# Performance work log

Measured on AMD Instinct MI355X. Metric: run time of the kernel, lower is better.

## Reference

```python
import jax, jax.numpy as jnp
import numpy as np

DIM = 3072
HEADS = 24
HEAD_DIM = 128
MLP_HIDDEN = 12288
SEQ = 2048
BATCH = 1
EPS = 1e-6


def setup_inputs() -> dict:
    key = jax.random.key(0)
    ks = jax.random.split(key, 12)
    s = 0.02
    return {
        "hidden_states": jax.random.normal(ks[0], (BATCH, SEQ, DIM), jnp.float32),
        "temb": jax.random.normal(ks[1], (BATCH, DIM), jnp.float32),
        "rope_cos": jax.random.uniform(ks[2], (SEQ, HEAD_DIM), jnp.float32),
        "rope_sin": jax.random.uniform(ks[3], (SEQ, HEAD_DIM), jnp.float32),
        # AdaLN-Zero single: Linear(dim -> 3*dim)
        "norm_w": jax.random.normal(ks[4], (3 * DIM, DIM), jnp.float32) * s,
        "norm_b": jnp.zeros((3 * DIM,), jnp.float32),
        # fused QKV + MLP projection: Linear(dim -> 3*dim + mlp_hidden)
        "qkv_mlp_w": jax.random.normal(ks[5], (3 * DIM + MLP_HIDDEN, DIM), jnp.float32) * s,
        "qkv_mlp_b": jnp.zeros((3 * DIM + MLP_HIDDEN,), jnp.float32),
        # proj_out: Linear(dim + mlp_hidden -> dim)
        "proj_w": jax.random.normal(ks[6], (DIM, DIM + MLP_HIDDEN), jnp.float32) * s,
        "proj_b": jnp.zeros((DIM,), jnp.float32),
        # qk RMSNorm weights (per head_dim)
        "rms_q_w": jnp.ones((HEAD_DIM,), jnp.float32),
        "rms_k_w": jnp.ones((HEAD_DIM,), jnp.float32),
    }


def _rms_norm(x, w):
    # x: [B,S,H,D], normalize over D
    var = jnp.mean(jnp.square(x), axis=-1, keepdims=True)
    return x * jax.lax.rsqrt(var + EPS) * w


def _apply_rope(x, cos, sin):
    # x: [B,S,H,D]; cos/sin: [S,D]. diffusers use_real, unbind_dim=-1 convention.
    xr = x.reshape(*x.shape[:-1], HEAD_DIM // 2, 2)
    rot = jnp.stack([-xr[..., 1], xr[..., 0]], axis=-1).reshape(x.shape)
    c = cos[None, :, None, :]
    s = sin[None, :, None, :]
    return x * c + rot * s


def reference(hidden_states, temb, rope_cos, rope_sin, norm_w, norm_b,
              qkv_mlp_w, qkv_mlp_b, proj_w, proj_b, rms_q_w, rms_k_w):
    B, S, _ = hidden_states.shape
    residual = hidden_states

    # --- AdaLayerNormZeroSingle ---
    mod = jax.nn.silu(temb) @ norm_w.T + norm_b          # [B, 3*dim]
    shift, scale, gate = jnp.split(mod, 3, axis=-1)       # each [B, dim]
    mu = jnp.mean(hidden_states, axis=-1, keepdims=True)
    var = jnp.mean(jnp.square(hidden_states - mu), axis=-1, keepdims=True)
    ln = (hidden_states - mu) * jax.lax.rsqrt(var + EPS)
    norm_h = ln * (1.0 + scale[:, None, :]) + shift[:, None, :]

    # --- fused QKV + MLP GEMM ---
    qkv_mlp = norm_h @ qkv_mlp_w.T + qkv_mlp_b             # [B,S,3*dim+mlp]
    qkv, mlp_h = jnp.split(qkv_mlp, [3 * DIM], axis=-1)
    mlp_out = jax.nn.gelu(mlp_h, approximate=True)         # tanh GELU

    q, k, v = jnp.split(qkv, 3, axis=-1)
    q = q.reshape(B, S, HEADS, HEAD_DIM)
    k = k.reshape(B, S, HEADS, HEAD_DIM)
    v = v.reshape(B, S, HEADS, HEAD_DIM)

    # qk RMSNorm + RoPE
    q = _apply_rope(_rms_norm(q, rms_q_w), rope_cos, rope_sin)
    k = _apply_rope(_rms_norm(k, rms_k_w), rope_cos, rope_sin)

    # scaled dot-product attention
    scale_f = 1.0 / np.sqrt(HEAD_DIM)
    scores = jnp.einsum("bqhd,bkhd->bhqk", q, k) * scale_f
    probs = jax.nn.softmax(scores, axis=-1)
    attn = jnp.einsum("bhqk,bkhd->bqhd", probs, v).reshape(B, S, DIM)

    # proj_out on concat(attn, gelu(mlp)) + gated residual
    cat = jnp.concatenate([attn, mlp_out], axis=-1)        # [B,S,dim+mlp]
    proj = cat @ proj_w.T + proj_b                          # [B,S,dim]
    return gate[:, None, :] * proj + residual
```

## Files before the change

### kernel.cpp

```cpp
#include <hip/hip_runtime.h>
#include <stdint.h>

typedef __bf16 bf16;
typedef __bf16 bf16x8 __attribute__((ext_vector_type(8)));
typedef __bf16 bf16x4 __attribute__((ext_vector_type(4)));
typedef float f32x4 __attribute__((ext_vector_type(4)));

#define DIM   3072
#define SEQ   2048
#define QKVW  9216
#define MLPH  12288
#define FUSED 21504
#define CATW  15360
#define HD    128
#define NH    24

__device__ __forceinline__ void gload_lds16(const void* g, void* l) {
  __builtin_amdgcn_global_load_lds((__attribute__((address_space(1))) void*)g,
                                   (__attribute__((address_space(3))) void*)l,
                                   16, 0, 0);
}

__global__ __launch_bounds__(256) void k_mod_gemv(
    const float* __restrict__ temb, const float* __restrict__ nw,
    const float* __restrict__ nb, float* __restrict__ mod)
{
  int j = blockIdx.x * 4 + (threadIdx.x >> 6);
  int lane = threadIdx.x & 63;
  const float* row = nw + (size_t)j * DIM;
  float acc = 0.f;
  #pragma unroll
  for (int k0 = 0; k0 < DIM; k0 += 256) {
    int k = k0 + lane * 4;
    float4 w = *(const float4*)(row + k);
    float4 t = *(const float4*)(temb + k);
    float s0 = t.x / (1.f + __expf(-t.x));
    float s1 = t.y / (1.f + __expf(-t.y));
    float s2 = t.z / (1.f + __expf(-t.z));
    float s3 = t.w / (1.f + __expf(-t.w));
    acc += w.x * s0 + w.y * s1 + w.z * s2 + w.w * s3;
  }
  #pragma unroll
  for (int m = 32; m >= 1; m >>= 1) acc += __shfl_xor(acc, m, 64);
  if (lane == 0) mod[j] = acc + nb[j];
}

__global__ __launch_bounds__(256) void k_ln_mod(
    const float* __restrict__ hs, const float* __restrict__ mod,
    bf16* __restrict__ nh)
{
  int m = blockIdx.x;
  int t = threadIdx.x;
  const float* x = hs + (size_t)m * DIM;
  float4 v[3];
  float s = 0.f, ss = 0.f;
  #pragma unroll
  for (int i = 0; i < 3; i++) {
    v[i] = *(const float4*)(x + i * 1024 + t * 4);
    s  += v[i].x + v[i].y + v[i].z + v[i].w;
    ss += v[i].x * v[i].x + v[i].y * v[i].y + v[i].z * v[i].z + v[i].w * v[i].w;
  }
  #pragma unroll
  for (int msk = 32; msk >= 1; msk >>= 1) {
    s  += __shfl_xor(s, msk, 64);
    ss += __shfl_xor(ss, msk, 64);
  }
  __shared__ float red[8];
  int wave = t >> 6;
  if ((t & 63) == 0) { red[wave] = s; red[4 + wave] = ss; }
  __syncthreads();
  s  = red[0] + red[1] + red[2] + red[3];
  ss = red[4] + red[5] + red[6] + red[7];
  float mu  = s * (1.f / DIM);
  float var = ss * (1.f / DIM) - mu * mu;
  float rstd = rsqrtf(var + 1e-6f);
  #pragma unroll
  for (int i = 0; i < 3; i++) {
    int col = i * 1024 + t * 4;
    const float* sc = mod + DIM + col;
    const float* sh = mod + col;
    float4 vv = v[i];
    bf16x4 o;
    o[0] = (bf16)((vv.x - mu) * rstd * (1.f + sc[0]) + sh[0]);
    o[1] = (bf16)((vv.y - mu) * rstd * (1.f + sc[1]) + sh[1]);
    o[2] = (bf16)((vv.z - mu) * rstd * (1.f + sc[2]) + sh[2]);
    o[3] = (bf16)((vv.w - mu) * rstd * (1.f + sc[3]) + sh[3]);
    *(bf16x4*)(nh + (size_t)m * DIM + col) = o;
  }
}

__global__ __launch_bounds__(256) void k_cvt(
    const float* __restrict__ s, bf16* __restrict__ d, size_t n)
{
  size_t stride = (size_t)gridDim.x * 256 * 8;
  for (size_t i = ((size_t)blockIdx.x * 256 + threadIdx.x) * 8; i < n; i += stride) {
    float4 a = *(const float4*)(s + i);
    float4 b = *(const float4*)(s + i + 4);
    bf16x8 h;
    h[0] = (bf16)a.x; h[1] = (bf16)a.y; h[2] = (bf16)a.z; h[3] = (bf16)a.w;
    h[4] = (bf16)b.x; h[5] = (bf16)b.y; h[6] = (bf16)b.z; h[7] = (bf16)b.w;
    *(bf16x8*)(d + i) = h;
  }
}

#define MFMA_B16(a, b, c) __builtin_amdgcn_mfma_f32_16x16x32_bf16(a, b, c, 0, 0, 0)

template<int MODE>
__global__ __launch_bounds__(512, 2) void k_gemm8(
    const bf16* __restrict__ A, const bf16* __restrict__ B,
    const float* __restrict__ bias, int K, int ntn, int nkp,
    bf16* __restrict__ oq, bf16* __restrict__ ocat, float* __restrict__ pk)
{
  __shared__ bf16 lds[65536];
  int tid = threadIdx.x;
  int wave = tid >> 6, lane = tid & 63;
  int wm = wave >> 2, wn = wave & 3;

  int nwg = gridDim.x;
  int bid = blockIdx.x;
  int swz = (bid & 7) * (nwg >> 3) + (bid >> 3);
  int mt = swz & 7;
  int rest = swz >> 3;
  int nt = rest % ntn;
  int kc = rest / ntn;
  int m0 = mt * 256, n0 = nt * 256;
  int Kp = K / nkp;
  int kbeg = kc * Kp;
  int NT = Kp >> 6;

  const bf16* Ag = A + (size_t)m0 * K + kbeg;
  const bf16* Bg = B + (size_t)n0 * K + kbeg;

  int aoffs[2][2], boffs[2][2];
  int aldc[2][2], bldc[2][2];
  #pragma unroll
  for (int q = 0; q < 2; q++) {
    #pragma unroll
    for (int j = 0; j < 2; j++) {
      int ca = j * 16 + q * 8 + wave;
      aoffs[q][j] = ((ca >> 1) * 16 + (lane & 15)) * K + (ca & 1) * 32 + (lane >> 4) * 8;
      aldc[q][j] = ca * 512;
      int v = j * 8 + wave;
      int cb = (v >> 2) * 8 + q * 4 + (v & 3);
      boffs[q][j] = ((cb >> 1) * 16 + (lane & 15)) * K + (cb & 1) * 32 + (lane >> 4) * 8;
      bldc[q][j] = 16384 + cb * 512;
    }
  }

  auto stA = [&](int kt, int q) {
    int kw = kt >= NT ? kt - NT : kt;
    int bo = (kt & 1) << 15;
    gload_lds16(Ag + aoffs[q][0] + kw * 64, &lds[bo + aldc[q][0]]);
    gload_lds16(Ag + aoffs[q][1] + kw * 64, &lds[bo + aldc[q][1]]);
  };
  auto stB = [&](int kt, int q) {
    int kw = kt >= NT ? kt - NT : kt;
    int bo = (kt & 1) << 15;
    gload_lds16(Bg + boffs[q][0] + kw * 64, &lds[bo + bldc[q][0]]);
    gload_lds16(Bg + boffs[q][1] + kw * 64, &lds[bo + bldc[q][1]]);
  };

  f32x4 acc[8][4];
  #pragma unroll
  for (int i = 0; i < 8; i++)
    #pragma unroll
    for (int j = 0; j < 4; j++) acc[i][j] = (f32x4){0.f, 0.f, 0.f, 0.f};

  const int abase = wm * 8192;
  const int bbase = 16384 + wn * 4096;
  const int lo = lane * 8;
  bf16x8 aLo[4][2], aHi[4][2], bLo[2][2], bHi[2][2];

  #define RD_ALO(BO) \
    _Pragma("unroll") for (int mi = 0; mi < 4; mi++) \
    _Pragma("unroll") for (int ks = 0; ks < 2; ks++) \
      aLo[mi][ks] = *(const bf16x8*)&lds[(BO) + abase + (mi * 2 + ks) * 512 + lo];
  #define RD_AHI(BO) \
    _Pragma("unroll") for (int mi = 0; mi < 4; mi++) \
    _Pragma("unroll") for (int ks = 0; ks < 2; ks++) \
      aHi[mi][ks] = *(const bf16x8*)&lds[(BO) + abase + ((4 + mi) * 2 + ks) * 512 + lo];
  #define RD_BLO(BO) \
    _Pragma("unroll") for (int ni = 0; ni < 2; ni++) \
    _Pragma("unroll") for (int ks = 0; ks < 2; ks++) \
      bLo[ni][ks] = *(const bf16x8*)&lds[(BO) + bbase + (ni * 2 + ks) * 512 + lo];
  #define RD_BHI(BO) \
    _Pragma("unroll") for (int ni = 0; ni < 2; ni++) \
    _Pragma("unroll") for (int ks = 0; ks < 2; ks++) \
      bHi[ni][ks] = *(const bf16x8*)&lds[(BO) + bbase + ((2 + ni) * 2 + ks) * 512 + lo];
  #define QUAD(AF, BF, MI0, NI0) \
    __builtin_amdgcn_s_setprio(1); \
    _Pragma("unroll") for (int mi = 0; mi < 4; mi++) \
    _Pragma("unroll") for (int ni = 0; ni < 2; ni++) \
    _Pragma("unroll") for (int ks = 0; ks < 2; ks++) \
      acc[MI0 + mi][NI0 + ni] = MFMA_B16(AF[mi][ks], BF[ni][ks], acc[MI0 + mi][NI0 + ni]); \
    __builtin_amdgcn_s_setprio(0);
  #define BAR()   __builtin_amdgcn_s_barrier()
  #define VM6()   asm volatile("s_waitcnt vmcnt(6)" ::: "memory")

  stA(0, 0); stB(0, 0); stA(0, 1); stB(0, 1);
  stA(1, 0); stB(1, 0); stA(1, 1);
  VM6();
  BAR();
  RD_ALO(0) RD_BLO(0)

  for (int it = 0; it < NT; it += 2) {
    int ta = it, tb = it + 1;
    BAR();
    stB(tb, 1);
    RD_AHI(0)
    QUAD(aLo, bLo, 0, 0)
    BAR();
    stA(ta + 2, 0);
    RD_BHI(0)
    QUAD(aHi, bLo, 4, 0)
    BAR();
    stB(ta + 2, 0);
    QUAD(aLo, bHi, 0, 2)
    stA(ta + 2, 1);
    VM6();
    BAR();
    RD_ALO(32768) RD_BLO(32768)
    QUAD(aHi, bHi, 4, 2)
    BAR();
    stB(ta + 2, 1);
    RD_AHI(32768)
    QUAD(aLo, bLo, 0, 0)
    BAR();
    stA(tb + 2, 0);
    RD_BHI(32768)
    QUAD(aHi, bLo, 4, 0)
    BAR();
    stB(tb + 2, 0);
    QUAD(aLo, bHi, 0, 2)
    stA(tb + 2, 1);
    VM6();
    BAR();
    RD_ALO(0) RD_BLO(0)
    QUAD(aHi, bHi, 4, 2)
  }

  int rr = (lane >> 4) * 4, cl = lane & 15;
  int mw0 = m0 + wm * 128, nw0 = n0 + wn * 64;
  #pragma unroll
  for (int mi = 0; mi < 8; mi++) {
    #pragma unroll
    for (int ni = 0; ni < 4; ni++) {
      int n = nw0 + ni * 16 + cl;
      #pragma unroll
      for (int r = 0; r < 4; r++) {
        int m = mw0 + mi * 16 + rr + r;
        float v = acc[mi][ni][r];
        if (MODE == 0) {
          v += bias[n];
          if (n < QKVW) {
            oq[(size_t)m * QKVW + n] = (bf16)v;
          } else {
            float g = 0.5f * v * (1.f + tanhf(0.7978845608028654f * (v + 0.044715f * v * v * v)));
            ocat[(size_t)m * CATW + DIM + (n - QKVW)] = (bf16)g;
          }
        } else {
          pk[(size_t)kc * SEQ * DIM + (size_t)m * DIM + n] = v;
        }
      }
    }
  }
  #undef RD_ALO
  #undef RD_AHI
  #undef RD_BLO
  #undef RD_BHI
  #undef QUAD
  #undef BAR
  #undef VM6
}

template<int MODE>
__global__ __launch_bounds__(256) void k_gemm2(
    const bf16* __restrict__ A, const float* __restrict__ Bf,
    const float* __restrict__ bias, int K, int ntn,
    bf16* __restrict__ oq, bf16* __restrict__ ocat,
    const float* __restrict__ gate, const float* __restrict__ resid,
    float* __restrict__ of)
{
  __shared__ bf16 sA[8192];
  __shared__ bf16 sB[8192];
  int nwg = gridDim.x;
  int bid = blockIdx.x;
  int swz = (bid & 7) * (nwg >> 3) + (bid >> 3);
  int mt = swz & 15, nt = swz >> 4;
  int m0 = mt * 128, n0 = nt * 128;
  int tid = threadIdx.x;
  int wave = tid >> 6, lane = tid & 63;
  int wr = wave >> 1, wc = wave & 1;

  size_t aoff[4], boff[4];
  bf16* la[4];
  bf16* lb[4];
  #pragma unroll
  for (int i = 0; i < 4; i++) {
    int c = wave * 4 + i;
    int rt = c >> 1, kt = c & 1;
    int row = rt * 16 + (lane & 15);
    int col = kt * 32 + (lane >> 4) * 8;
    aoff[i] = (size_t)(m0 + row) * K + col;
    boff[i] = (size_t)(n0 + row) * K + col;
    la[i] = sA + c * 512;
    lb[i] = sB + c * 512;
  }
  f32x4 acc[4][4];
  #pragma unroll
  for (int i = 0; i < 4; i++)
    #pragma unroll
    for (int j = 0; j < 4; j++) acc[i][j] = (f32x4){0.f, 0.f, 0.f, 0.f};

  for (int kk = 0; kk < K; kk += 64) {
    #pragma unroll
    for (int i = 0; i < 4; i++)
      gload_lds16(A + aoff[i] + kk, la[i]);
    #pragma unroll
    for (int i = 0; i < 4; i++) {
      const float* g = Bf + boff[i] + kk;
      float4 f0 = *(const float4*)g;
      float4 f1 = *(const float4*)(g + 4);
      bf16x8 h;
      h[0] = (bf16)f0.x; h[1] = (bf16)f0.y; h[2] = (bf16)f0.z; h[3] = (bf16)f0.w;
      h[4] = (bf16)f1.x; h[5] = (bf16)f1.y; h[6] = (bf16)f1.z; h[7] = (bf16)f1.w;
      *(bf16x8*)(lb[i] + lane * 8) = h;
    }
    __syncthreads();
    #pragma unroll
    for (int ks = 0; ks < 2; ks++) {
      bf16x8 af[4], bfr[4];
      #pragma unroll
      for (int mi = 0; mi < 4; mi++)
        af[mi] = *(const bf16x8*)(sA + ((wr * 4 + mi) * 2 + ks) * 512 + lane * 8);
      #pragma unroll
      for (int nj = 0; nj < 4; nj++)
        bfr[nj] = *(const bf16x8*)(sB + ((wc * 4 + nj) * 2 + ks) * 512 + lane * 8);
      #pragma unroll
      for (int mi = 0; mi < 4; mi++)
        #pragma unroll
        for (int nj = 0; nj < 4; nj++)
          acc[mi][nj] = __builtin_amdgcn_mfma_f32_16x16x32_bf16(af[mi], bfr[nj], acc[mi][nj], 0, 0, 0);
    }
    __syncthreads();
  }

  int rr = (lane >> 4) * 4;
  int cl = lane & 15;
  #pragma unroll
  for (int mi = 0; mi < 4; mi++) {
    #pragma unroll
    for (int nj = 0; nj < 4; nj++) {
      int mbase = m0 + wr * 64 + mi * 16 + rr;
      int n = n0 + wc * 64 + nj * 16 + cl;
      #pragma unroll
      for (int r = 0; r < 4; r++) {
        int m = mbase + r;
        float v = acc[mi][nj][r] + bias[n];
        if (MODE == 0) {
          if (n < QKVW) {
            oq[(size_t)m * QKVW + n] = (bf16)v;
          } else {
            float g = 0.5f * v * (1.f + tanhf(0.7978845608028654f * (v + 0.044715f * v * v * v)));
            ocat[(size_t)m * CATW + DIM + (n - QKVW)] = (bf16)g;
          }
        } else {
          of[(size_t)m * DIM + n] = gate[n] * v + resid[(size_t)m * DIM + n];
        }
      }
    }
  }
}

__global__ __launch_bounds__(256) void k_red(
    const float* __restrict__ pk, const float* __restrict__ bias,
    const float* __restrict__ gate, const float* __restrict__ resid,
    float* __restrict__ out)
{
  int m = blockIdx.x / 3;
  int n = (blockIdx.x % 3) * 1024 + threadIdx.x * 4;
  size_t idx = (size_t)m * DIM + n;
  f32x4 p0 = *(const f32x4*)(pk + idx);
  f32x4 p1 = *(const f32x4*)(pk + (size_t)SEQ * DIM + idx);
  f32x4 b  = *(const f32x4*)(bias + n);
  f32x4 g  = *(const f32x4*)(gate + n);
  f32x4 r  = *(const f32x4*)(resid + idx);
  f32x4 o;
  #pragma unroll
  for (int i = 0; i < 4; i++) o[i] = g[i] * (p0[i] + p1[i] + b[i]) + r[i];
  *(f32x4*)(out + idx) = o;
}

__global__ __launch_bounds__(256) void k_rmsrope(
    bf16* __restrict__ qkv, const float* __restrict__ rc, const float* __restrict__ rs,
    const float* __restrict__ qw, const float* __restrict__ kw)
{
  int srow = blockIdx.x >> 1;
  int isk  = blockIdx.x & 1;
  int off  = isk ? DIM : 0;
  const float* w = isk ? kw : qw;
  int g = threadIdx.x >> 5, gl = threadIdx.x & 31;
  int d = gl * 4;
  #pragma unroll
  for (int hh = 0; hh < 3; hh++) {
    int h = g + hh * 8;
    bf16* p = qkv + (size_t)srow * QKVW + off + h * HD + d;
    bf16x4 u = *(const bf16x4*)p;
    float x0 = (float)u[0], x1 = (float)u[1], x2 = (float)u[2], x3 = (float)u[3];
    float ssq = x0 * x0 + x1 * x1 + x2 * x2 + x3 * x3;
    #pragma unroll
    for (int msk = 16; msk >= 1; msk >>= 1) ssq += __shfl_xor(ssq, msk, 32);
    float r = rsqrtf(ssq * (1.f / HD) + 1e-6f);
    float y0 = x0 * r * w[d], y1 = x1 * r * w[d + 1];
    float y2 = x2 * r * w[d + 2], y3 = x3 * r * w[d + 3];
    const float* c = rc + srow * HD + d;
    const float* sn = rs + srow * HD + d;
    bf16x4 o;
    o[0] = (bf16)(y0 * c[0] - y1 * sn[0]);
    o[1] = (bf16)(y1 * c[1] + y0 * sn[1]);
    o[2] = (bf16)(y2 * c[2] - y3 * sn[2]);
    o[3] = (bf16)(y3 * c[3] + y2 * sn[3]);
    *(bf16x4*)p = o;
  }
}

__global__ __launch_bounds__(256) void k_attn(
    const bf16* __restrict__ qkv, bf16* __restrict__ cat)
{
  int h  = blockIdx.y;
  int q0 = blockIdx.x * 64;
  int tid = threadIdx.x, wave = tid >> 6, lane = tid & 63;
  int r16 = lane & 15, g4 = lane >> 4;
  __shared__ bf16 sK[32 * 168];
  __shared__ bf16 sVt[128 * 40];
  __shared__ bf16 sP[4][16 * 40];

  bf16x8 qf[4];
  {
    int qrow = q0 + wave * 16 + r16;
    const bf16* qp = qkv + (size_t)qrow * QKVW + h * HD + g4 * 8;
    #pragma unroll
    for (int kc = 0; kc < 4; kc++) qf[kc] = *(const bf16x8*)(qp + kc * 32);
  }
  f32x4 oacc[8];
  #pragma unroll
  for (int dc = 0; dc < 8; dc++) oacc[dc] = (f32x4){0.f, 0.f, 0.f, 0.f};
  float mrow[4] = {-1e30f, -1e30f, -1e30f, -1e30f};
  float lrow[4] = {0.f, 0.f, 0.f, 0.f};
  const float scale = 0.08838834764831845f;

  int krow = tid >> 3, c0 = (tid & 7) * 16;
  const bf16* kbase = qkv + (size_t)krow * QKVW + DIM + h * HD + c0;
  const bf16* vbase = qkv + (size_t)krow * QKVW + 2 * DIM + h * HD + c0;

  bf16x8 kr0 = *(const bf16x8*)(kbase);
  bf16x8 kr1 = *(const bf16x8*)(kbase + 8);
  bf16x8 vr0 = *(const bf16x8*)(vbase);
  bf16x8 vr1 = *(const bf16x8*)(vbase + 8);

  for (int kv0 = 0; kv0 < SEQ; kv0 += 32) {
    *(bf16x8*)&sK[krow * 168 + c0]     = kr0;
    *(bf16x8*)&sK[krow * 168 + c0 + 8] = kr1;
    #pragma unroll
    for (int i = 0; i < 8; i++) {
      sVt[(c0 + i) * 40 + krow]     = vr0[i];
      sVt[(c0 + 8 + i) * 40 + krow] = vr1[i];
    }
    __syncthreads();
    if (kv0 + 32 < SEQ) {
      const bf16* kn = kbase + (size_t)(kv0 + 32) * QKVW;
      const bf16* vn = vbase + (size_t)(kv0 + 32) * QKVW;
      kr0 = *(const bf16x8*)(kn);
      kr1 = *(const bf16x8*)(kn + 8);
      vr0 = *(const bf16x8*)(vn);
      vr1 = *(const bf16x8*)(vn + 8);
    }

    f32x4 sv[2];
    sv[0] = (f32x4){0.f, 0.f, 0.f, 0.f};
    sv[1] = (f32x4){0.f, 0.f, 0.f, 0.f};
    #pragma unroll
    for (int ct = 0; ct < 2; ct++)
      #pragma unroll
      for (int kc = 0; kc < 4; kc++) {
        bf16x8 kf = *(const bf16x8*)&sK[(ct * 16 + r16) * 168 + kc * 32 + g4 * 8];
        sv[ct] = __builtin_amdgcn_mfma_f32_16x16x32_bf16(qf[kc], kf, sv[ct], 0, 0, 0);
      }

    bf16* sPw = &sP[wave][0];
    #pragma unroll
    for (int r = 0; r < 4; r++) {
      float a0 = sv[0][r] * scale, a1 = sv[1][r] * scale;
      float mx = fmaxf(a0, a1);
      #pragma unroll
      for (int msk = 8; msk >= 1; msk >>= 1) mx = fmaxf(mx, __shfl_xor(mx, msk, 16));
      float mnew = fmaxf(mrow[r], mx);
      float so = __expf(mrow[r] - mnew);
      float p0 = __expf(a0 - mnew), p1 = __expf(a1 - mnew);
      float rsum = p0 + p1;
      #pragma unroll
      for (int msk = 8; msk >= 1; msk >>= 1) rsum += __shfl_xor(rsum, msk, 16);
      lrow[r] = lrow[r] * so + rsum;
      mrow[r] = mnew;
      #pragma unroll
      for (int dc = 0; dc < 8; dc++) oacc[dc][r] *= so;
      int prow = g4 * 4 + r;
      sPw[prow * 40 + r16]      = (bf16)p0;
      sPw[prow * 40 + 16 + r16] = (bf16)p1;
    }
    asm volatile("s_waitcnt lgkmcnt(0)" ::: "memory");
    __builtin_amdgcn_sched_barrier(0);
    bf16x8 pa = *(const bf16x8*)&sPw[r16 * 40 + g4 * 8];
    #pragma unroll
    for (int dc = 0; dc < 8; dc++) {
      bf16x8 vf = *(const bf16x8*)&sVt[(dc * 16 + r16) * 40 + g4 * 8];
      oacc[dc] = __builtin_amdgcn_mfma_f32_16x16x32_bf16(pa, vf, oacc[dc], 0, 0, 0);
    }
    __syncthreads();
  }

  #pragma unroll
  for (int dc = 0; dc < 8; dc++) {
    #pragma unroll
    for (int r = 0; r < 4; r++) {
      int qrow = q0 + wave * 16 + g4 * 4 + r;
      int col  = h * HD + dc * 16 + r16;
      cat[(size_t)qrow * CATW + col] = (bf16)(oacc[dc][r] / lrow[r]);
    }
  }
}

extern "C" void kernel_launch(void* const* d_in, const int* in_sizes, int n_in,
                              void* d_out, int out_size, void* d_ws, size_t ws_size,
                              hipStream_t stream) {
  const float* hs      = (const float*)d_in[0];
  const float* temb    = (const float*)d_in[1];
  const float* rope_c  = (const float*)d_in[2];
  const float* rope_s  = (const float*)d_in[3];
  const float* norm_w  = (const float*)d_in[4];
  const float* norm_b  = (const float*)d_in[5];
  const float* qkvml_w = (const float*)d_in[6];
  const float* qkvml_b = (const float*)d_in[7];
  const float* proj_w  = (const float*)d_in[8];
  const float* proj_b  = (const float*)d_in[9];
  const float* rms_q_w = (const float*)d_in[10];
  const float* rms_k_w = (const float*)d_in[11];
  float* out = (float*)d_out;

  char* ws = (char*)d_ws;
  size_t off = 0;
  float* mod  = (float*)(ws + off); off += 40960;
  bf16*  nh   = (bf16*)(ws + off); off += (size_t)SEQ * DIM * 2;
  bf16*  qkvb = (bf16*)(ws + off); off += (size_t)SEQ * QKVW * 2;
  bf16*  catb = (bf16*)(ws + off); off += (size_t)SEQ * CATW * 2;
  bf16*  wqb  = (bf16*)(ws + off); off += (size_t)FUSED * DIM * 2;
  bf16*  wpb  = (bf16*)(ws + off); off += (size_t)DIM * CATW * 2;
  float* pkbf = (float*)(ws + off); off += (size_t)2 * SEQ * DIM * 4;
  bool full = (ws_size >= off);

  if (full) {
    k_cvt<<<dim3(2048), dim3(256), 0, stream>>>(qkvml_w, wqb, (size_t)FUSED * DIM);
    k_cvt<<<dim3(2048), dim3(256), 0, stream>>>(proj_w, wpb, (size_t)DIM * CATW);
  }
  k_mod_gemv<<<dim3(QKVW / 4), dim3(256), 0, stream>>>(temb, norm_w, norm_b, mod);
  k_ln_mod<<<dim3(SEQ), dim3(256), 0, stream>>>(hs, mod, nh);

  if (full) {
    k_gemm8<0><<<dim3(8 * (FUSED / 256)), dim3(512), 0, stream>>>(
        nh, wqb, qkvml_b, DIM, FUSED / 256, 1, qkvb, catb, nullptr);
  } else {
    k_gemm2<0><<<dim3(16 * (FUSED / 128)), dim3(256), 0, stream>>>(
        nh, qkvml_w, qkvml_b, DIM, FUSED / 128, qkvb, catb, nullptr, nullptr, nullptr);
  }

  k_rmsrope<<<dim3(SEQ * 2), dim3(256), 0, stream>>>(qkvb, rope_c, rope_s, rms_q_w, rms_k_w);
  k_attn<<<dim3(SEQ / 64, NH), dim3(256), 0, stream>>>(qkvb, catb);

  if (full) {
    k_gemm8<1><<<dim3(8 * (DIM / 256) * 2), dim3(512), 0, stream>>>(
        catb, wpb, nullptr, CATW, DIM / 256, 2, nullptr, nullptr, pkbf);
    k_red<<<dim3(SEQ * 3), dim3(256), 0, stream>>>(pkbf, proj_b, mod + 2 * DIM, hs, out);
  } else {
    k_gemm2<1><<<dim3(16 * (DIM / 128)), dim3(256), 0, stream>>>(
        catb, proj_w, proj_b, CATW, DIM / 128, nullptr, nullptr, mod + 2 * DIM, hs, out);
  }
}
```

Measured before the change: 1.069 ms.

## Replace 256x256 8-wave GEMM with 128x128 4-wave tile and simpler pipeline

Measured after the change: 1.329 ms. 24.4% more time.

```diff
diff --git a/kernel.cpp b/kernel.cpp
--- a/kernel.cpp
+++ b/kernel.cpp
@@ -106,24 +106,24 @@
 #define MFMA_B16(a, b, c) __builtin_amdgcn_mfma_f32_16x16x32_bf16(a, b, c, 0, 0, 0)
 
 template<int MODE>
-__global__ __launch_bounds__(512, 2) void k_gemm8(
+__global__ __launch_bounds__(256, 2) void k_gemm4(
     const bf16* __restrict__ A, const bf16* __restrict__ B,
     const float* __restrict__ bias, int K, int ntn, int nkp,
     bf16* __restrict__ oq, bf16* __restrict__ ocat, float* __restrict__ pk)
 {
-  __shared__ bf16 lds[65536];
+  __shared__ bf16 lds[32768];
   int tid = threadIdx.x;
   int wave = tid >> 6, lane = tid & 63;
-  int wm = wave >> 2, wn = wave & 3;
+  int wr = wave >> 1, wc = wave & 1;
 
   int nwg = gridDim.x;
   int bid = blockIdx.x;
   int swz = (bid & 7) * (nwg >> 3) + (bid >> 3);
-  int mt = swz & 7;
-  int rest = swz >> 3;
+  int mt = swz & 15;
+  int rest = swz >> 4;
   int nt = rest % ntn;
   int kc = rest / ntn;
-  int m0 = mt * 256, n0 = nt * 256;
+  int m0 = mt * 128, n0 = nt * 128;
   int Kp = K / nkp;
   int kbeg = kc * Kp;
   int NT = Kp >> 6;
@@ -131,118 +131,74 @@
   const bf16* Ag = A + (size_t)m0 * K + kbeg;
   const bf16* Bg = B + (size_t)n0 * K + kbeg;
 
-  int aoffs[2][2], boffs[2][2];
-  int aldc[2][2], bldc[2][2];
-  #pragma unroll
-  for (int q = 0; q < 2; q++) {
+  int goff[2][2];
+  #pragma unroll
+  for (int h = 0; h < 2; h++)
     #pragma unroll
     for (int j = 0; j < 2; j++) {
-      int ca = j * 16 + q * 8 + wave;
-      aoffs[q][j] = ((ca >> 1) * 16 + (lane & 15)) * K + (ca & 1) * 32 + (lane >> 4) * 8;
-      aldc[q][j] = ca * 512;
-      int v = j * 8 + wave;
-      int cb = (v >> 2) * 8 + q * 4 + (v & 3);
-      boffs[q][j] = ((cb >> 1) * 16 + (lane & 15)) * K + (cb & 1) * 32 + (lane >> 4) * 8;
-      bldc[q][j] = 16384 + cb * 512;
-    }
-  }
-
-  auto stA = [&](int kt, int q) {
+      int c = h * 8 + j * 4 + wave;
+      goff[h][j] = ((c & 7) * 16 + (lane & 15)) * K + h * 32 + (lane >> 4) * 8;
+    }
+
+  auto STG = [&](int kt, int h) {
     int kw = kt >= NT ? kt - NT : kt;
-    int bo = (kt & 1) << 15;
-    gload_lds16(Ag + aoffs[q][0] + kw * 64, &lds[bo + aldc[q][0]]);
-    gload_lds16(Ag + aoffs[q][1] + kw * 64, &lds[bo + aldc[q][1]]);
+    int bo = (kt & 1) << 14;
+    #pragma unroll
+    for (int j = 0; j < 2; j++) {
+      int c = h * 8 + j * 4 + wave;
+      gload_lds16(Ag + goff[h][j] + kw * 64, &lds[bo + c * 512]);
+      gload_lds16(Bg + goff[h][j] + kw * 64, &lds[bo + 8192 + c * 512]);
+    }
   };
-  auto stB = [&](int kt, int q) {
-    int kw = kt >= NT ? kt - NT : kt;
-    int bo = (kt & 1) << 15;
-    gload_lds16(Bg + boffs[q][0] + kw * 64, &lds[bo + bldc[q][0]]);
-    gload_lds16(Bg + boffs[q][1] + kw * 64, &lds[bo + bldc[q][1]]);
-  };
-
-  f32x4 acc[8][4];
-  #pragma unroll
-  for (int i = 0; i < 8; i++)
+
+  f32x4 acc[4][4];
+  #pragma unroll
+  for (int i = 0; i < 4; i++)
     #pragma unroll
     for (int j = 0; j < 4; j++) acc[i][j] = (f32x4){0.f, 0.f, 0.f, 0.f};
 
-  const int abase = wm * 8192;
-  const int bbase = 16384 + wn * 4096;
   const int lo = lane * 8;
-  bf16x8 aLo[4][2], aHi[4][2], bLo[2][2], bHi[2][2];
-
-  #define RD_ALO(BO) \
+  bf16x8 af[4], bfr[4];
+
+  #define BAR()   __builtin_amdgcn_s_barrier()
+  #define LGKM0() asm volatile("s_waitcnt lgkmcnt(0)" ::: "memory")
+  #define VM8()   asm volatile("s_waitcnt vmcnt(8)" ::: "memory")
+  #define SB0()   __builtin_amdgcn_sched_barrier(0)
+  #define RD(KS, BO) \
     _Pragma("unroll") for (int mi = 0; mi < 4; mi++) \
-    _Pragma("unroll") for (int ks = 0; ks < 2; ks++) \
-      aLo[mi][ks] = *(const bf16x8*)&lds[(BO) + abase + (mi * 2 + ks) * 512 + lo];
-  #define RD_AHI(BO) \
-    _Pragma("unroll") for (int mi = 0; mi < 4; mi++) \
-    _Pragma("unroll") for (int ks = 0; ks < 2; ks++) \
-      aHi[mi][ks] = *(const bf16x8*)&lds[(BO) + abase + ((4 + mi) * 2 + ks) * 512 + lo];
-  #define RD_BLO(BO) \
-    _Pragma("unroll") for (int ni = 0; ni < 2; ni++) \
-    _Pragma("unroll") for (int ks = 0; ks < 2; ks++) \
-      bLo[ni][ks] = *(const bf16x8*)&lds[(BO) + bbase + (ni * 2 + ks) * 512 + lo];
-  #define RD_BHI(BO) \
-    _Pragma("unroll") for (int ni = 0; ni < 2; ni++) \
-    _Pragma("unroll") for (int ks = 0; ks < 2; ks++) \
-      bHi[ni][ks] = *(const bf16x8*)&lds[(BO) + bbase + ((2 + ni) * 2 + ks) * 512 + lo];
-  #define QUAD(AF, BF, MI0, NI0) \
+      af[mi] = *(const bf16x8*)&lds[(BO) + ((KS) * 8 + wr * 4 + mi) * 512 + lo]; \
+    _Pragma("unroll") for (int ni = 0; ni < 4; ni++) \
+      bfr[ni] = *(const bf16x8*)&lds[(BO) + 8192 + ((KS) * 8 + wc * 4 + ni) * 512 + lo];
+  #define QUAD() \
     __builtin_amdgcn_s_setprio(1); \
     _Pragma("unroll") for (int mi = 0; mi < 4; mi++) \
-    _Pragma("unroll") for (int ni = 0; ni < 2; ni++) \
-    _Pragma("unroll") for (int ks = 0; ks < 2; ks++) \
-      acc[MI0 + mi][NI0 + ni] = MFMA_B16(AF[mi][ks], BF[ni][ks], acc[MI0 + mi][NI0 + ni]); \
+    _Pragma("unroll") for (int ni = 0; ni < 4; ni++) \
+      acc[mi][ni] = MFMA_B16(af[mi], bfr[ni], acc[mi][ni]); \
     __builtin_amdgcn_s_setprio(0);
-  #define BAR()   __builtin_amdgcn_s_barrier()
-  #define VM6()   asm volatile("s_waitcnt vmcnt(6)" ::: "memory")
-
-  stA(0, 0); stB(0, 0); stA(0, 1); stB(0, 1);
-  stA(1, 0); stB(1, 0); stA(1, 1);
-  VM6();
+
+  STG(0, 0); STG(0, 1); STG(1, 0);
+  VM8();
   BAR();
-  RD_ALO(0) RD_BLO(0)
-
-  for (int it = 0; it < NT; it += 2) {
-    int ta = it, tb = it + 1;
+  for (int t = 0; t < NT; t++) {
+    int bo = (t & 1) << 14;
+    RD(0, bo)
+    STG(t + 1, 1);
+    VM8();
+    BAR(); LGKM0(); SB0();
+    QUAD()
     BAR();
-    stB(tb, 1);
-    RD_AHI(0)
-    QUAD(aLo, bLo, 0, 0)
+    RD(1, bo)
+    STG(t + 2, 0);
+    VM8();
+    BAR(); LGKM0(); SB0();
+    QUAD()
     BAR();
-    stA(ta + 2, 0);
-    RD_BHI(0)
-    QUAD(aHi, bLo, 4, 0)
-    BAR();
-    stB(ta + 2, 0);
-    QUAD(aLo, bHi, 0, 2)
-    stA(ta + 2, 1);
-    VM6();
-    BAR();
-    RD_ALO(32768) RD_BLO(32768)
-    QUAD(aHi, bHi, 4, 2)
-    BAR();
-    stB(ta + 2, 1);
-    RD_AHI(32768)
-    QUAD(aLo, bLo, 0, 0)
-    BAR();
-    stA(tb + 2, 0);
-    RD_BHI(32768)
-    QUAD(aHi, bLo, 4, 0)
-    BAR();
-    stB(tb + 2, 0);
-    QUAD(aLo, bHi, 0, 2)
-    stA(tb + 2, 1);
-    VM6();
-    BAR();
-    RD_ALO(0) RD_BLO(0)
-    QUAD(aHi, bHi, 4, 2)
   }
 
   int rr = (lane >> 4) * 4, cl = lane & 15;
-  int mw0 = m0 + wm * 128, nw0 = n0 + wn * 64;
-  #pragma unroll
-  for (int mi = 0; mi < 8; mi++) {
+  int mw0 = m0 + wr * 64, nw0 = n0 + wc * 64;
+  #pragma unroll
+  for (int mi = 0; mi < 4; mi++) {
     #pragma unroll
     for (int ni = 0; ni < 4; ni++) {
       int n = nw0 + ni * 16 + cl;
@@ -264,13 +220,12 @@
       }
     }
   }
-  #undef RD_ALO
-  #undef RD_AHI
-  #undef RD_BLO
-  #undef RD_BHI
+  #undef BAR
+  #undef LGKM0
+  #undef VM8
+  #undef SB0
+  #undef RD
   #undef QUAD
-  #undef BAR
-  #undef VM6
 }
 
 template<int MODE>
@@ -375,19 +330,23 @@
 __global__ __launch_bounds__(256) void k_red(
     const float* __restrict__ pk, const float* __restrict__ bias,
     const float* __restrict__ gate, const float* __restrict__ resid,
-    float* __restrict__ out)
+    float* __restrict__ out, int parts)
 {
   int m = blockIdx.x / 3;
   int n = (blockIdx.x % 3) * 1024 + threadIdx.x * 4;
   size_t idx = (size_t)m * DIM + n;
-  f32x4 p0 = *(const f32x4*)(pk + idx);
-  f32x4 p1 = *(const f32x4*)(pk + (size_t)SEQ * DIM + idx);
+  f32x4 s = *(const f32x4*)(pk + idx);
+  for (int p = 1; p < parts; p++) {
+    f32x4 q = *(const f32x4*)(pk + (size_t)p * SEQ * DIM + idx);
+    #pragma unroll
+    for (int i = 0; i < 4; i++) s[i] += q[i];
+  }
   f32x4 b  = *(const f32x4*)(bias + n);
   f32x4 g  = *(const f32x4*)(gate + n);
   f32x4 r  = *(const f32x4*)(resid + idx);
   f32x4 o;
   #pragma unroll
-  for (int i = 0; i < 4; i++) o[i] = g[i] * (p0[i] + p1[i] + b[i]) + r[i];
+  for (int i = 0; i < 4; i++) o[i] = g[i] * (s[i] + b[i]) + r[i];
   *(f32x4*)(out + idx) = o;
 }
 
@@ -566,8 +525,8 @@
   k_ln_mod<<<dim3(SEQ), dim3(256), 0, stream>>>(hs, mod, nh);
 
   if (full) {
-    k_gemm8<0><<<dim3(8 * (FUSED / 256)), dim3(512), 0, stream>>>(
-        nh, wqb, qkvml_b, DIM, FUSED / 256, 1, qkvb, catb, nullptr);
+    k_gemm4<0><<<dim3(16 * (FUSED / 128)), dim3(256), 0, stream>>>(
+        nh, wqb, qkvml_b, DIM, FUSED / 128, 1, qkvb, catb, nullptr);
   } else {
     k_gemm2<0><<<dim3(16 * (FUSED / 128)), dim3(256), 0, stream>>>(
         nh, qkvml_w, qkvml_b, DIM, FUSED / 128, qkvb, catb, nullptr, nullptr, nullptr);
@@ -577,9 +536,9 @@
   k_attn<<<dim3(SEQ / 64, NH), dim3(256), 0, stream>>>(qkvb, catb);
 
   if (full) {
-    k_gemm8<1><<<dim3(8 * (DIM / 256) * 2), dim3(512), 0, stream>>>(
-        catb, wpb, nullptr, CATW, DIM / 256, 2, nullptr, nullptr, pkbf);
-    k_red<<<dim3(SEQ * 3), dim3(256), 0, stream>>>(pkbf, proj_b, mod + 2 * DIM, hs, out);
+    k_gemm4<1><<<dim3(16 * (DIM / 128) * 2), dim3(256), 0, stream>>>(
+        catb, wpb, nullptr, CATW, DIM / 128, 2, nullptr, nullptr, pkbf);
+    k_red<<<dim3(SEQ * 3), dim3(256), 0, stream>>>(pkbf, proj_b, mod + 2 * DIM, hs, out, 2);
   } else {
     k_gemm2<1><<<dim3(16 * (DIM / 128)), dim3(256), 0, stream>>>(
         catb, proj_w, proj_b, CATW, DIM / 128, nullptr, nullptr, mod + 2 * DIM, hs, out);
```
